# Optimization experiments

Measured on AMD Instinct MI355X. Metric: run time of the kernel, lower is better.

Reference implementation:

```python
import jax, jax.numpy as jnp
import numpy as np

T, D_MODEL, D_FF, N_EXPERTS, TOP_K = 8192, 1024, 4096, 8, 2

def setup_inputs() -> dict:
    key = jax.random.key(0)
    k1, k2, k3, k4, k5 = jax.random.split(key, 5)
    hidden_states = jax.random.normal(k1, (T, D_MODEL), dtype=jnp.float32)
    # router picks TOP_K distinct-ish experts per token; build one-hot mask [T, K, E]
    expert_idx = jax.random.randint(k2, (T, TOP_K), 0, N_EXPERTS)
    selected_experts = jax.nn.one_hot(expert_idx, N_EXPERTS, dtype=jnp.int32)
    rw = jax.random.uniform(k3, (T, TOP_K), dtype=jnp.float32)
    routing_weights = rw / jnp.sum(rw, axis=-1, keepdims=True)
    scale = 1.0 / np.sqrt(D_MODEL)
    wi = jax.random.normal(k4, (N_EXPERTS, D_FF, D_MODEL), dtype=jnp.float32) * scale
    wo = jax.random.normal(k5, (N_EXPERTS, D_MODEL, D_FF), dtype=jnp.float32) * (1.0 / np.sqrt(D_FF))
    return {"hidden_states": hidden_states, "selected_experts": selected_experts,
            "routing_weights": routing_weights, "wi": wi, "wo": wo}

def reference(hidden_states, selected_experts, routing_weights, wi, wo):
    # expert_mask: [E, K, T] (as in torch permute(2,1,0))
    mask = jnp.transpose(selected_experts, (2, 1, 0)).astype(hidden_states.dtype)
    # combined per-token weight for each expert: w[t, e] = sum_k mask[e,k,t]*routing_weights[t,k]
    w = jnp.einsum('ekt,tk->te', mask, routing_weights)
    out = jnp.zeros_like(hidden_states)
    # fixed small loop over experts; tokens not routed to expert e get weight 0,
    # so this is mathematically identical to the gather->MLP->scale->scatter-add.
    for e in range(wi.shape[0]):
        h = jax.nn.relu(hidden_states @ wi[e].T)     # [T, d_ff] (dropout is identity at eval)
        y = h @ wo[e].T                              # [T, d_model]
        out = out + w[:, e:e + 1] * y
    return out
```

## Files before the change

### kernel.cpp

```cpp
#include <hip/hip_runtime.h>
#include <hip/hip_bf16.h>


#define T_TOK   8192
#define D_MODEL 1024
#define D_FF    4096
#define NE      8
#define MT2     72
#define ROWS_MAX (MT2 * 256)
#define BUF1    32768
#define LDS_G1  65536
#define BUF2    24576
#define LDS_G2  49152

typedef float f32x4 __attribute__((ext_vector_type(4)));
typedef short s16x8 __attribute__((ext_vector_type(8)));
typedef short s16x4 __attribute__((ext_vector_type(4)));
typedef unsigned short u16;

__device__ __forceinline__ u16 f2bf(float x) {
  __hip_bfloat16 h = __float2bfloat16(x);
  return *reinterpret_cast<u16*>(&h);
}

__device__ __forceinline__ s16x8 cvt8(float4 a, float4 b) {
  s16x8 v;
  v[0] = (short)f2bf(a.x); v[1] = (short)f2bf(a.y);
  v[2] = (short)f2bf(a.z); v[3] = (short)f2bf(a.w);
  v[4] = (short)f2bf(b.x); v[5] = (short)f2bf(b.y);
  v[6] = (short)f2bf(b.z); v[7] = (short)f2bf(b.w);
  return v;
}

__device__ __forceinline__ void gload_lds16(const void* g, void* l) {
  __builtin_amdgcn_global_load_lds((const __attribute__((address_space(1))) void*)g,
                                   (__attribute__((address_space(3))) void*)l,
                                   16, 0, 0);
}

__global__ void moe_route(const int* __restrict__ sel, const float* __restrict__ rw,
                          int* __restrict__ cnt, int* __restrict__ tidx,
                          float* __restrict__ tw) {
  int t = blockIdx.x * blockDim.x + threadIdx.x;
  if (t >= T_TOK) return;
  int e0 = 0, e1 = 0;
  #pragma unroll
  for (int e = 0; e < NE; ++e) {
    if (sel[t * 16 + e])     e0 = e;
    if (sel[t * 16 + 8 + e]) e1 = e;
  }
  float w0 = rw[2 * t], w1 = rw[2 * t + 1];
  if (e0 == e1) {
    int p = atomicAdd(&cnt[e0], 1);
    tidx[e0 * T_TOK + p] = t; tw[e0 * T_TOK + p] = w0 + w1;
  } else {
    int p = atomicAdd(&cnt[e0], 1);
    tidx[e0 * T_TOK + p] = t; tw[e0 * T_TOK + p] = w0;
    int q = atomicAdd(&cnt[e1], 1);
    tidx[e1 * T_TOK + q] = t; tw[e1 * T_TOK + q] = w1;
  }
}

__global__ void moe_tilemap(const int* __restrict__ cnt, const int* __restrict__ tidx,
                            const float* __restrict__ tw, int* __restrict__ te256,
                            int* __restrict__ tokr, float* __restrict__ wr) {
  int off[NE + 1];
  {
    int o = 0;
    #pragma unroll
    for (int e = 0; e < NE; ++e) { off[e] = o; o += (cnt[e] + 255) & ~255; }
    off[NE] = o;
  }
  const int total = off[NE];
  const int gid = blockIdx.x * blockDim.x + threadIdx.x;
  const int stride = gridDim.x * blockDim.x;
  for (int t = gid; t < MT2; t += stride) {
    int r0 = t * 256; int e = -1;
    if (r0 < total) {
      #pragma unroll
      for (int i = NE - 1; i >= 0; --i) if (r0 >= off[i]) { e = i; break; }
    }
    te256[t] = e;
  }
  for (int i = gid; i < ROWS_MAX; i += stride) {
    if (i >= total) { tokr[i] = -1; wr[i] = 0.f; continue; }
    int e = 0;
    #pragma unroll
    for (int k = NE - 1; k >= 0; --k) if (i >= off[k]) { e = k; break; }
    int j = i - off[e];
    int ok = j < cnt[e];
    tokr[i] = ok ? tidx[e * T_TOK + j] : -1;
    wr[i]   = ok ? tw[e * T_TOK + j] : 0.f;
  }
}

__global__ void moe_gather_x(const float* __restrict__ hs, const int* __restrict__ tokr,
                             u16* __restrict__ Xg) {
  int row = blockIdx.x;
  int tok = tokr[row];
  int c = threadIdx.x * 4;
  u16* dst = Xg + (size_t)row * D_MODEL + c;
  s16x4 o;
  if (tok < 0) {
    o[0] = o[1] = o[2] = o[3] = 0;
  } else {
    float4 v = *(const float4*)(hs + (size_t)tok * D_MODEL + c);
    o[0] = (short)f2bf(v.x); o[1] = (short)f2bf(v.y);
    o[2] = (short)f2bf(v.z); o[3] = (short)f2bf(v.w);
  }
  *(s16x4*)dst = o;
}

__global__ void moe_cvt_w(const float* __restrict__ wi, const float* __restrict__ wo,
                          u16* __restrict__ wib, u16* __restrict__ wob) {
  const size_t NW = (size_t)NE * D_FF * D_MODEL;
  size_t i = ((size_t)blockIdx.x * blockDim.x + threadIdx.x) * 8;
  const float* src; u16* dst;
  if (i < NW) { src = wi + i; dst = wib + i; }
  else        { src = wo + (i - NW); dst = wob + (i - NW); }
  float4 a = *(const float4*)(src);
  float4 b = *(const float4*)(src + 4);
  *(s16x8*)dst = cvt8(a, b);
}

__global__ void moe_cvt_wi_s(const float* __restrict__ wi, u16* __restrict__ wis,
                             int W, int f0) {
  size_t i = ((size_t)blockIdx.x * blockDim.x + threadIdx.x) * 8;
  size_t per = (size_t)W * D_MODEL;
  int e = (int)(i / per); size_t r = i % per;
  const float* src = wi + ((size_t)e * D_FF + f0) * D_MODEL + r;
  float4 a = *(const float4*)src;
  float4 b = *(const float4*)(src + 4);
  *(s16x8*)(wis + i) = cvt8(a, b);
}

__global__ void moe_cvt_wo_s(const float* __restrict__ wo, u16* __restrict__ wos,
                             int W, int f0) {
  size_t i = ((size_t)blockIdx.x * blockDim.x + threadIdx.x) * 8;
  size_t per = (size_t)D_MODEL * W;
  int e = (int)(i / per); size_t r = i % per;
  int row = (int)(r / W), col = (int)(r % W);
  const float* src = wo + ((size_t)e * D_MODEL + row) * D_FF + f0 + col;
  float4 a = *(const float4*)src;
  float4 b = *(const float4*)(src + 4);
  *(s16x8*)(wos + i) = cvt8(a, b);
}

#define MM4(mi, a) \
  acc[mi][0] = __builtin_amdgcn_mfma_f32_16x16x32_bf16(a, bq0, acc[mi][0], 0, 0, 0); \
  acc[mi][1] = __builtin_amdgcn_mfma_f32_16x16x32_bf16(a, bq1, acc[mi][1], 0, 0, 0); \
  acc[mi][2] = __builtin_amdgcn_mfma_f32_16x16x32_bf16(a, bq2, acc[mi][2], 0, 0, 0); \
  acc[mi][3] = __builtin_amdgcn_mfma_f32_16x16x32_bf16(a, bq3, acc[mi][3], 0, 0, 0);

template <bool FULL>
__global__ __launch_bounds__(512, 2)
void moe_g1(const u16* __restrict__ Xg, const u16* __restrict__ wiP,
            const int* __restrict__ te256, u16* __restrict__ H,
            int W, int f0) {
  extern __shared__ char lds[];
  const int GR = gridDim.x;
  const int task = (blockIdx.x & 7) * (GR >> 3) + (blockIdx.x >> 3);
  const int mt = task % MT2;
  const int nc = task / MT2;
  const int e = te256[mt];
  if (e < 0) return;
  const int grow0 = mt * 256;
  const int fcol = nc * 256;

  const int tid = threadIdx.x;
  const int lane = tid & 63, wv = tid >> 6;
  const int lg = lane >> 4, ll = lane & 15;
  const int wm = wv >> 2, wn = wv & 3;

  const int sw = (tid * 16) ^ (((tid >> 3) & 7) << 4);
  const int srow = sw >> 6, scol = sw & 63;
  const int inner = (ll * 64 + lg * 16) ^ (((ll >> 1) & 7) << 4);

  const char* gA = (const char*)(Xg + (size_t)grow0 * D_MODEL);
  const char* gB = (const char*)(wiP + (FULL ? ((size_t)e * D_FF + f0 + fcol)
                                             : ((size_t)e * W + fcol)) * D_MODEL);

  f32x4 acc[8][4];
  #pragma unroll
  for (int m = 0; m < 8; ++m)
    #pragma unroll
    for (int n = 0; n < 4; ++n) acc[m][n] = (f32x4){0.f, 0.f, 0.f, 0.f};

  auto stage = [&](int kb, char* lbuf) {
    #pragma unroll
    for (int j = 0; j < 2; ++j)
      gload_lds16(gA + (size_t)(j * 128 + srow) * 2048 + kb + scol,
                  lbuf + j * 8192 + tid * 16);
    #pragma unroll
    for (int j = 0; j < 2; ++j)
      gload_lds16(gB + (size_t)(j * 128 + srow) * 2048 + kb + scol,
                  lbuf + 16384 + j * 8192 + tid * 16);
  };

  const int NT = D_MODEL / 32;
  stage(0, lds);
  stage(64, lds + BUF1);
  for (int t = 0; t < NT; ++t) {
    if (t < NT - 1) { asm volatile("s_waitcnt vmcnt(4)" ::: "memory"); }
    else            { asm volatile("s_waitcnt vmcnt(0)" ::: "memory"); }
    asm volatile("s_barrier" ::: "memory");
    char* lbuf = lds + (t & 1) * BUF1;
    const char* la = lbuf + wm * 8192;
    const char* lb = lbuf + 16384 + wn * 4096;
    s16x8 bq0 = *(const s16x8*)(lb + 0 * 1024 + inner);
    s16x8 bq1 = *(const s16x8*)(lb + 1 * 1024 + inner);
    s16x8 bq2 = *(const s16x8*)(lb + 2 * 1024 + inner);
    s16x8 bq3 = *(const s16x8*)(lb + 3 * 1024 + inner);
    {
      s16x8 a0 = *(const s16x8*)(la + 0 * 1024 + inner);
      s16x8 a1 = *(const s16x8*)(la + 1 * 1024 + inner);
      s16x8 a2 = *(const s16x8*)(la + 2 * 1024 + inner);
      s16x8 a3 = *(const s16x8*)(la + 3 * 1024 + inner);
      __builtin_amdgcn_s_setprio(1);
      MM4(0, a0) MM4(1, a1) MM4(2, a2) MM4(3, a3)
      __builtin_amdgcn_s_setprio(0);
    }
    {
      s16x8 a0 = *(const s16x8*)(la + 4 * 1024 + inner);
      s16x8 a1 = *(const s16x8*)(la + 5 * 1024 + inner);
      s16x8 a2 = *(const s16x8*)(la + 6 * 1024 + inner);
      s16x8 a3 = *(const s16x8*)(la + 7 * 1024 + inner);
      __builtin_amdgcn_s_setprio(1);
      MM4(4, a0) MM4(5, a1) MM4(6, a2) MM4(7, a3)
      __builtin_amdgcn_s_setprio(0);
    }
    asm volatile("s_barrier" ::: "memory");
    if (t + 2 < NT) stage((t + 2) * 64, lbuf);
  }

  #pragma unroll
  for (int mf = 0; mf < 8; ++mf) {
    #pragma unroll
    for (int r = 0; r < 4; ++r) {
      int row = grow0 + wm * 128 + mf * 16 + lg * 4 + r;
      u16* hp = H + (size_t)row * W + fcol + wn * 64 + ll;
      #pragma unroll
      for (int nf = 0; nf < 4; ++nf) {
        float v = acc[mf][nf][r];
        hp[nf * 16] = f2bf(v > 0.f ? v : 0.f);
      }
    }
  }
}

template <bool FULL>
__global__ __launch_bounds__(512, 3)
void moe_g2(const u16* __restrict__ H, const u16* __restrict__ woP,
            const int* __restrict__ te256, const int* __restrict__ tokr,
            const float* __restrict__ wr, float* __restrict__ out,
            int W, int f0, int KCH) {
  extern __shared__ char lds[];
  const int GR = gridDim.x;
  const int task = (blockIdx.x & 7) * (GR >> 3) + (blockIdx.x >> 3);
  const int dc = task & 7;
  const int rest = task >> 3;
  const int mt = rest % MT2;
  const int kc = rest / MT2;
  const int e = te256[mt];
  if (e < 0) return;
  const int grow0 = mt * 256;
  const int dcol0 = dc * 128;

  const int tid = threadIdx.x;
  const int lane = tid & 63, wv = tid >> 6;
  const int lg = lane >> 4, ll = lane & 15;
  const int wm = wv >> 1, wn = wv & 1;

  const int sw = (tid * 16) ^ (((tid >> 3) & 7) << 4);
  const int srow = sw >> 6, scol = sw & 63;
  const int inner = (ll * 64 + lg * 16) ^ (((ll >> 1) & 7) << 4);

  const size_t pA = (size_t)W * 2;
  const size_t pB = (FULL ? (size_t)D_FF : (size_t)W) * 2;
  const char* gA = (const char*)(H + (size_t)grow0 * W) + (size_t)kc * KCH * 2;
  const char* gB = (const char*)(woP + ((size_t)e * D_MODEL + dcol0) * (pB / 2)
                                 + (FULL ? f0 : 0)) + (size_t)kc * KCH * 2;

  f32x4 acc[4][4];
  #pragma unroll
  for (int m = 0; m < 4; ++m)
    #pragma unroll
    for (int n = 0; n < 4; ++n) acc[m][n] = (f32x4){0.f, 0.f, 0.f, 0.f};

  auto stage = [&](int kb, char* lbuf) {
    #pragma unroll
    for (int j = 0; j < 2; ++j)
      gload_lds16(gA + (size_t)(j * 128 + srow) * pA + kb + scol,
                  lbuf + j * 8192 + tid * 16);
    gload_lds16(gB + (size_t)srow * pB + kb + scol, lbuf + 16384 + tid * 16);
  };

  const int NT = KCH / 32;
  stage(0, lds);
  stage(64, lds + BUF2);
  for (int t = 0; t < NT; ++t) {
    if (t < NT - 1) { asm volatile("s_waitcnt vmcnt(3)" ::: "memory"); }
    else            { asm volatile("s_waitcnt vmcnt(0)" ::: "memory"); }
    asm volatile("s_barrier" ::: "memory");
    char* lbuf = lds + (t & 1) * BUF2;
    const char* la = lbuf + wm * 4096;
    const char* lb = lbuf + 16384 + wn * 4096;
    s16x8 bq0 = *(const s16x8*)(lb + 0 * 1024 + inner);
    s16x8 bq1 = *(const s16x8*)(lb + 1 * 1024 + inner);
    s16x8 bq2 = *(const s16x8*)(lb + 2 * 1024 + inner);
    s16x8 bq3 = *(const s16x8*)(lb + 3 * 1024 + inner);
    {
      s16x8 a0 = *(const s16x8*)(la + 0 * 1024 + inner);
      s16x8 a1 = *(const s16x8*)(la + 1 * 1024 + inner);
      __builtin_amdgcn_s_setprio(1);
      MM4(0, a0) MM4(1, a1)
      __builtin_amdgcn_s_setprio(0);
    }
    {
      s16x8 a2 = *(const s16x8*)(la + 2 * 1024 + inner);
      s16x8 a3 = *(const s16x8*)(la + 3 * 1024 + inner);
      __builtin_amdgcn_s_setprio(1);
      MM4(2, a2) MM4(3, a3)
      __builtin_amdgcn_s_setprio(0);
    }
    asm volatile("s_barrier" ::: "memory");
    if (t + 2 < NT) stage((t + 2) * 64, lbuf);
  }

  #pragma unroll
  for (int mf = 0; mf < 4; ++mf) {
    #pragma unroll
    for (int r = 0; r < 4; ++r) {
      int row = grow0 + wm * 64 + mf * 16 + lg * 4 + r;
      int tok = tokr[row];
      if (tok >= 0) {
        float w = wr[row];
        float* op = out + (size_t)tok * D_MODEL + dcol0 + wn * 64 + ll;
        #pragma unroll
        for (int nf = 0; nf < 4; ++nf)
          atomicAdd(op + nf * 16, acc[mf][nf][r] * w);
      }
    }
  }
}

extern "C" void kernel_launch(void* const* d_in, const int* in_sizes, int n_in,
                              void* d_out, int out_size, void* d_ws, size_t ws_size,
                              hipStream_t stream) {
  const float* hs  = (const float*)d_in[0];
  const int*   sel = (const int*)d_in[1];
  const float* rw  = (const float*)d_in[2];
  const float* wi  = (const float*)d_in[3];
  const float* wo  = (const float*)d_in[4];
  float* out = (float*)d_out;

  const size_t NW   = (size_t)NE * D_FF * D_MODEL;
  const size_t CTRL = 1u << 20;
  const size_t WB   = 2 * NW * sizeof(u16);
  const size_t XGB  = (size_t)ROWS_MAX * D_MODEL * 2;

  bool FULLW = true; int W = D_FF;
  {
    bool found = false;
    for (int f : {1, 2, 4, 8, 16}) {
      int Wc = D_FF / f;
      size_t need = CTRL + WB + XGB + (size_t)ROWS_MAX * Wc * 2;
      if (need <= ws_size) { FULLW = true; W = Wc; found = true; break; }
    }
    if (!found) {
      for (int Wc : {1024, 512, 256}) {
        size_t sl = (size_t)2 * NE * Wc * D_MODEL * 2;
        size_t need = CTRL + sl + XGB + (size_t)ROWS_MAX * Wc * 2;
        if (need <= ws_size) { FULLW = false; W = Wc; break; }
      }
    }
  }
  const int FS = D_FF / W;

  size_t off = 0;
  auto take = [&](size_t b) -> char* {
    char* r = (char*)d_ws + off; off = (off + b + 255) & ~(size_t)255; return r;
  };
  int*   tidx = (int*)take((size_t)NE * T_TOK * 4);
  float* tw   = (float*)take((size_t)NE * T_TOK * 4);
  int*   tokr = (int*)take((size_t)ROWS_MAX * 4);
  float* wrr  = (float*)take((size_t)ROWS_MAX * 4);
  int*   te2  = (int*)take(MT2 * 4);
  int*   cnt  = (int*)take(256);
  off = CTRL;
  u16 *wiP, *woP;
  if (FULLW) { wiP = (u16*)take(NW * 2); woP = (u16*)take(NW * 2); }
  else       { wiP = (u16*)take((size_t)NE * W * D_MODEL * 2);
               woP = (u16*)take((size_t)NE * D_MODEL * W * 2); }
  u16* Xg   = (u16*)take(XGB);
  u16* Hbuf = (u16*)take((size_t)ROWS_MAX * W * 2);

  hipMemsetAsync(cnt, 0, 256, stream);
  hipMemsetAsync(d_out, 0, (size_t)out_size * sizeof(float), stream);
  moe_route<<<T_TOK / 256, 256, 0, stream>>>(sel, rw, cnt, tidx, tw);
  moe_tilemap<<<64, 256, 0, stream>>>(cnt, tidx, tw, te2, tokr, wrr);
  moe_gather_x<<<ROWS_MAX, 256, 0, stream>>>(hs, tokr, Xg);
  if (FULLW)
    moe_cvt_w<<<(int)(2 * NW / 8 / 256), 256, 0, stream>>>(wi, wo, wiP, woP);

  hipFuncSetAttribute(reinterpret_cast<const void*>(&moe_g1<true>),
                      hipFuncAttributeMaxDynamicSharedMemorySize, LDS_G1);
  hipFuncSetAttribute(reinterpret_cast<const void*>(&moe_g1<false>),
                      hipFuncAttributeMaxDynamicSharedMemorySize, LDS_G1);
  hipFuncSetAttribute(reinterpret_cast<const void*>(&moe_g2<true>),
                      hipFuncAttributeMaxDynamicSharedMemorySize, LDS_G2);
  hipFuncSetAttribute(reinterpret_cast<const void*>(&moe_g2<false>),
                      hipFuncAttributeMaxDynamicSharedMemorySize, LDS_G2);

  const int KCH = W / 2;
  const int g1grid = MT2 * (W / 256);
  const int g2grid = MT2 * 8 * 2;
  const int cvtblk = (int)(((size_t)NE * W * D_MODEL / 8) / 256);

  for (int p = 0; p < FS; ++p) {
    const int f0 = p * W;
    if (!FULLW) {
      moe_cvt_wi_s<<<cvtblk, 256, 0, stream>>>(wi, wiP, W, f0);
      moe_cvt_wo_s<<<cvtblk, 256, 0, stream>>>(wo, woP, W, f0);
    }
    if (FULLW) {
      moe_g1<true><<<g1grid, 512, LDS_G1, stream>>>(Xg, wiP, te2, Hbuf, W, f0);
      moe_g2<true><<<g2grid, 512, LDS_G2, stream>>>(Hbuf, woP, te2, tokr, wrr,
                                                    out, W, f0, KCH);
    } else {
      moe_g1<false><<<g1grid, 512, LDS_G1, stream>>>(Xg, wiP, te2, Hbuf, W, f0);
      moe_g2<false><<<g2grid, 512, LDS_G2, stream>>>(Hbuf, woP, te2, tokr, wrr,
                                                     out, W, f0, KCH);
    }
  }
}
```

Measured before the change: 557.2 us.

## Triple-buffer LDS in both MoE GEMMs and interleave prefetch with MFMAs

```diff
diff --git a/kernel.cpp b/kernel.cpp
--- a/kernel.cpp
+++ b/kernel.cpp
@@ -8,10 +8,10 @@
 #define NE      8
 #define MT2     72
 #define ROWS_MAX (MT2 * 256)
-#define BUF1    32768
-#define LDS_G1  65536
+#define BUFB    32768
+#define LDS_G1  98304
 #define BUF2    24576
-#define LDS_G2  49152
+#define LDS_G2  73728
 
 typedef float f32x4 __attribute__((ext_vector_type(4)));
 typedef short s16x8 __attribute__((ext_vector_type(8)));
@@ -153,7 +153,7 @@
   acc[mi][3] = __builtin_amdgcn_mfma_f32_16x16x32_bf16(a, bq3, acc[mi][3], 0, 0, 0);
 
 template <bool FULL>
-__global__ __launch_bounds__(512, 2)
+__global__ __launch_bounds__(512, 1)
 void moe_g1(const u16* __restrict__ Xg, const u16* __restrict__ wiP,
             const int* __restrict__ te256, u16* __restrict__ H,
             int W, int f0) {
@@ -186,11 +186,13 @@
     #pragma unroll
     for (int n = 0; n < 4; ++n) acc[m][n] = (f32x4){0.f, 0.f, 0.f, 0.f};
 
-  auto stage = [&](int kb, char* lbuf) {
+  auto stageA = [&](int kb, char* lbuf) {
     #pragma unroll
     for (int j = 0; j < 2; ++j)
       gload_lds16(gA + (size_t)(j * 128 + srow) * 2048 + kb + scol,
                   lbuf + j * 8192 + tid * 16);
+  };
+  auto stageB = [&](int kb, char* lbuf) {
     #pragma unroll
     for (int j = 0; j < 2; ++j)
       gload_lds16(gB + (size_t)(j * 128 + srow) * 2048 + kb + scol,
@@ -198,15 +200,17 @@
   };
 
   const int NT = D_MODEL / 32;
-  stage(0, lds);
-  stage(64, lds + BUF1);
+  stageA(0, lds);   stageB(0, lds);
+  stageA(64, lds + BUFB); stageB(64, lds + BUFB);
+  int bufi = 0;
   for (int t = 0; t < NT; ++t) {
     if (t < NT - 1) { asm volatile("s_waitcnt vmcnt(4)" ::: "memory"); }
     else            { asm volatile("s_waitcnt vmcnt(0)" ::: "memory"); }
     asm volatile("s_barrier" ::: "memory");
-    char* lbuf = lds + (t & 1) * BUF1;
-    const char* la = lbuf + wm * 8192;
-    const char* lb = lbuf + 16384 + wn * 4096;
+    const char* la = lds + bufi * BUFB + wm * 8192;
+    const char* lb = lds + bufi * BUFB + 16384 + wn * 4096;
+    int b2 = bufi + 2; if (b2 >= 3) b2 -= 3;
+    const bool pf = (t + 2 < NT);
     s16x8 bq0 = *(const s16x8*)(lb + 0 * 1024 + inner);
     s16x8 bq1 = *(const s16x8*)(lb + 1 * 1024 + inner);
     s16x8 bq2 = *(const s16x8*)(lb + 2 * 1024 + inner);
@@ -216,6 +220,7 @@
       s16x8 a1 = *(const s16x8*)(la + 1 * 1024 + inner);
       s16x8 a2 = *(const s16x8*)(la + 2 * 1024 + inner);
       s16x8 a3 = *(const s16x8*)(la + 3 * 1024 + inner);
+      if (pf) stageA((t + 2) * 64, lds + b2 * BUFB);
       __builtin_amdgcn_s_setprio(1);
       MM4(0, a0) MM4(1, a1) MM4(2, a2) MM4(3, a3)
       __builtin_amdgcn_s_setprio(0);
@@ -225,12 +230,12 @@
       s16x8 a1 = *(const s16x8*)(la + 5 * 1024 + inner);
       s16x8 a2 = *(const s16x8*)(la + 6 * 1024 + inner);
       s16x8 a3 = *(const s16x8*)(la + 7 * 1024 + inner);
+      if (pf) stageB((t + 2) * 64, lds + b2 * BUFB);
       __builtin_amdgcn_s_setprio(1);
       MM4(4, a0) MM4(5, a1) MM4(6, a2) MM4(7, a3)
       __builtin_amdgcn_s_setprio(0);
     }
-    asm volatile("s_barrier" ::: "memory");
-    if (t + 2 < NT) stage((t + 2) * 64, lbuf);
+    bufi += 1; if (bufi >= 3) bufi -= 3;
   }
 
   #pragma unroll
@@ -249,7 +254,7 @@
 }
 
 template <bool FULL>
-__global__ __launch_bounds__(512, 3)
+__global__ __launch_bounds__(512, 4)
 void moe_g2(const u16* __restrict__ H, const u16* __restrict__ woP,
             const int* __restrict__ te256, const int* __restrict__ tokr,
             const float* __restrict__ wr, float* __restrict__ out,
@@ -287,24 +292,28 @@
     #pragma unroll
     for (int n = 0; n < 4; ++n) acc[m][n] = (f32x4){0.f, 0.f, 0.f, 0.f};
 
-  auto stage = [&](int kb, char* lbuf) {
+  auto stageA = [&](int kb, char* lbuf) {
     #pragma unroll
     for (int j = 0; j < 2; ++j)
       gload_lds16(gA + (size_t)(j * 128 + srow) * pA + kb + scol,
                   lbuf + j * 8192 + tid * 16);
+  };
+  auto stageB = [&](int kb, char* lbuf) {
     gload_lds16(gB + (size_t)srow * pB + kb + scol, lbuf + 16384 + tid * 16);
   };
 
   const int NT = KCH / 32;
-  stage(0, lds);
-  stage(64, lds + BUF2);
+  stageA(0, lds);   stageB(0, lds);
+  stageA(64, lds + BUF2); stageB(64, lds + BUF2);
+  int bufi = 0;
   for (int t = 0; t < NT; ++t) {
     if (t < NT - 1) { asm volatile("s_waitcnt vmcnt(3)" ::: "memory"); }
     else            { asm volatile("s_waitcnt vmcnt(0)" ::: "memory"); }
     asm volatile("s_barrier" ::: "memory");
-    char* lbuf = lds + (t & 1) * BUF2;
-    const char* la = lbuf + wm * 4096;
-    const char* lb = lbuf + 16384 + wn * 4096;
+    const char* la = lds + bufi * BUF2 + wm * 4096;
+    const char* lb = lds + bufi * BUF2 + 16384 + wn * 4096;
+    int b2 = bufi + 2; if (b2 >= 3) b2 -= 3;
+    const bool pf = (t + 2 < NT);
     s16x8 bq0 = *(const s16x8*)(lb + 0 * 1024 + inner);
     s16x8 bq1 = *(const s16x8*)(lb + 1 * 1024 + inner);
     s16x8 bq2 = *(const s16x8*)(lb + 2 * 1024 + inner);
@@ -312,6 +321,7 @@
     {
       s16x8 a0 = *(const s16x8*)(la + 0 * 1024 + inner);
       s16x8 a1 = *(const s16x8*)(la + 1 * 1024 + inner);
+      if (pf) stageA((t + 2) * 64, lds + b2 * BUF2);
       __builtin_amdgcn_s_setprio(1);
       MM4(0, a0) MM4(1, a1)
       __builtin_amdgcn_s_setprio(0);
@@ -319,12 +329,12 @@
     {
       s16x8 a2 = *(const s16x8*)(la + 2 * 1024 + inner);
       s16x8 a3 = *(const s16x8*)(la + 3 * 1024 + inner);
+      if (pf) stageB((t + 2) * 64, lds + b2 * BUF2);
       __builtin_amdgcn_s_setprio(1);
       MM4(2, a2) MM4(3, a3)
       __builtin_amdgcn_s_setprio(0);
     }
-    asm volatile("s_barrier" ::: "memory");
-    if (t + 2 < NT) stage((t + 2) * 64, lbuf);
+    bufi += 1; if (bufi >= 3) bufi -= 3;
   }
 
   #pragma unroll
```

Result: faster. 524.6 us (-5.9%).
